# Kernel optimization log

Measured on AMD Instinct MI355X. Metric: run time of the kernel, lower is better.

## Reference

```python
import jax, jax.numpy as jnp
import numpy as np

H, I, E, TOP_K = 2048, 8192, 8, 2
B, S = 2, 2048


def setup_inputs() -> dict:
    key = jax.random.key(0)
    k1, k2, k3, k4 = jax.random.split(key, 4)
    scale_h = 1.0 / np.sqrt(H)
    scale_i = 1.0 / np.sqrt(I)
    return {
        "hidden_states": jax.random.normal(k1, (B, S, H), dtype=jnp.float32),
        "gate_w": jax.random.normal(k2, (H, E), dtype=jnp.float32) * scale_h,
        "w_in": jax.random.normal(k3, (E, H, I), dtype=jnp.float32) * scale_h,
        "w_out": jax.random.normal(k4, (E, I, H), dtype=jnp.float32) * scale_i,
        "bias": jnp.zeros((H,), dtype=jnp.float32),
        "top_k": TOP_K,
    }


def reference(hidden_states, gate_w, w_in, w_out, bias, top_k):
    b, s, h = hidden_states.shape
    x = hidden_states.reshape(-1, h)                      # [T, H]
    num_experts = gate_w.shape[1]

    router_logits = x @ gate_w                            # [T, E]
    probs = jax.nn.softmax(router_logits.astype(jnp.float32), axis=-1)
    routing_weights, selected = jax.lax.top_k(probs, top_k)  # [T, K]
    # normalize_expert_weights=True
    routing_weights = routing_weights / routing_weights.sum(axis=-1, keepdims=True)
    routing_weights = routing_weights.astype(x.dtype)

    # per-token combine weight for each expert (0 if not selected)
    one_hot = jax.nn.one_hot(selected, num_experts, dtype=x.dtype)  # [T, K, E]
    combine = jnp.einsum('tk,tke->te', routing_weights, one_hot)    # [T, E]

    out = jnp.zeros_like(x)
    for e in range(num_experts):  # small fixed expert loop
        hmid = jax.nn.gelu(x @ w_in[e], approximate=False)  # [T, I]
        out = out + combine[:, e:e + 1] * (hmid @ w_out[e])  # [T, H]

    out = out.reshape(b, s, h) + bias
    return out, router_logits
```

## Files before the change

### kernel.cpp

```cpp
#include <hip/hip_runtime.h>
#include <hip/hip_bf16.h>
#include <math.h>

#define T_TOK 4096
#define H_DIM 2048
#define I_DIM 8192
#define N_EXP 8
#define NPAIR 8192

typedef short bf16x8 __attribute__((ext_vector_type(8)));
typedef float f32x4 __attribute__((ext_vector_type(4)));

__device__ __forceinline__ ushort f2bf(float f) {
    union { float f; unsigned u; } v; v.f = f;
    unsigned u = v.u + 0x7fffu + ((v.u >> 16) & 1u);
    return (ushort)(u >> 16);
}

__global__ void k_init(float* __restrict__ out, const float* __restrict__ bias,
                       int* __restrict__ cnts) {
    int gid = blockIdx.x * 256 + threadIdx.x;
    size_t i = (size_t)gid * 4;
    if (i < (size_t)T_TOK * H_DIM) {
        float4 b = *(const float4*)&bias[i & (H_DIM - 1)];
        *(float4*)&out[i] = b;
    }
    if (gid < 16) cnts[gid] = 0;
}

__global__ void k_cvt_x(const float* __restrict__ x, ushort* __restrict__ xb) {
    size_t i = ((size_t)blockIdx.x * 256 + threadIdx.x) * 4;
    float4 v = *(const float4*)&x[i];
    ushort4 o;
    o.x = f2bf(v.x); o.y = f2bf(v.y); o.z = f2bf(v.z); o.w = f2bf(v.w);
    *(ushort4*)&xb[i] = o;
}

__global__ void k_router(const float* __restrict__ x, const float* __restrict__ gw,
                         float* __restrict__ logits, int* __restrict__ sel,
                         float* __restrict__ wts, int* __restrict__ cnt) {
    int t = blockIdx.x;
    int lane = threadIdx.x;
    const float* xr = x + (size_t)t * H_DIM;
    float s[8] = {0, 0, 0, 0, 0, 0, 0, 0};
    for (int h = lane; h < H_DIM; h += 64) {
        float xv = xr[h];
        const float* g = gw + h * 8;
        float4 g0 = *(const float4*)g;
        float4 g1 = *(const float4*)(g + 4);
        s[0] += xv * g0.x; s[1] += xv * g0.y; s[2] += xv * g0.z; s[3] += xv * g0.w;
        s[4] += xv * g1.x; s[5] += xv * g1.y; s[6] += xv * g1.z; s[7] += xv * g1.w;
    }
#pragma unroll
    for (int off = 32; off > 0; off >>= 1) {
#pragma unroll
        for (int e = 0; e < 8; e++) s[e] += __shfl_xor(s[e], off);
    }
    if (lane < 8) logits[t * 8 + lane] = s[lane];
    if (lane == 0) {
        int e0 = 0; float l0 = s[0];
        for (int e = 1; e < 8; e++) if (s[e] > l0) { l0 = s[e]; e0 = e; }
        int e1 = -1; float l1 = -3.0e38f;
        for (int e = 0; e < 8; e++) if (e != e0 && s[e] > l1) { l1 = s[e]; e1 = e; }
        float w0 = 1.0f / (1.0f + expf(l1 - l0));
        float w1 = 1.0f - w0;
        sel[t * 2] = e0; sel[t * 2 + 1] = e1;
        wts[t * 2] = w0; wts[t * 2 + 1] = w1;
        atomicAdd(&cnt[e0], 1);
        atomicAdd(&cnt[e1], 1);
    }
}

__global__ void k_prefix(const int* __restrict__ cnt, int* __restrict__ offs) {
    if (threadIdx.x == 0 && blockIdx.x == 0) {
        int a = 0;
        for (int e = 0; e < N_EXP; e++) { offs[e] = a; a += cnt[e]; }
        offs[N_EXP] = a;
    }
}

__global__ void k_assign(const int* __restrict__ sel, const float* __restrict__ wts,
                         const int* __restrict__ offs, int* __restrict__ cursor,
                         int* __restrict__ rowinfo, float* __restrict__ rowwt) {
    int t = blockIdx.x * 256 + threadIdx.x;
    if (t >= T_TOK) return;
#pragma unroll
    for (int k = 0; k < 2; k++) {
        int e = sel[t * 2 + k];
        int pos = atomicAdd(&cursor[e], 1);
        int row = offs[e] + pos;
        rowinfo[row] = t;
        rowwt[row] = wts[t * 2 + k];
    }
}

template <int KDIM, int NDIM, int MODE>
__global__ __launch_bounds__(256) void k_gemm(
    const ushort* __restrict__ Abase, const float* __restrict__ Bbase,
    void* __restrict__ outp, const int* __restrict__ rowinfo,
    const float* __restrict__ rowwt, const int* __restrict__ offs) {
    const int e = blockIdx.z;
    const int row_start = offs[e], row_end = offs[e + 1];
    const int row0 = row_start + blockIdx.y * 128;
    if (row0 >= row_end) return;
    const int n0 = blockIdx.x * 128;
    const float* B = Bbase + (size_t)e * KDIM * NDIM;

    __shared__ ushort lds_a[128 * 56];
    __shared__ ushort lds_b[128 * 56];

    const int tid = threadIdx.x;
    const int ar = tid & 127;
    const int ak = (tid >> 7) << 4;
    int r = row0 + ar;
    int rc = (r < row_end) ? r : row_start;
    const ushort* a_src;
    if (MODE == 0) a_src = Abase + (size_t)rowinfo[rc] * KDIM + ak;
    else           a_src = Abase + (size_t)rc * KDIM + ak;
    ushort* a_dst = &lds_a[ar * 56 + ak];

    const int bn = (tid & 31) * 4;
    const int bk = (tid >> 5) * 4;
    const float* b_src = B + (size_t)bk * NDIM + (n0 + bn);

    const int lane = tid & 63;
    const int wid = tid >> 6;
    const int wm = (wid & 1) * 64;
    const int wn = (wid >> 1) * 64;
    const int l15 = lane & 15;
    const int q8 = (lane >> 4) * 8;

    f32x4 acc[4][4] = {};

    for (int k0 = 0; k0 < KDIM; k0 += 32) {
        uint4 av0 = *(const uint4*)(a_src + k0);
        uint4 av1 = *(const uint4*)(a_src + k0 + 8);
        const float* bs = b_src + (size_t)k0 * NDIM;
        float4 b0 = *(const float4*)(bs);
        float4 b1 = *(const float4*)(bs + NDIM);
        float4 b2 = *(const float4*)(bs + 2 * (size_t)NDIM);
        float4 b3 = *(const float4*)(bs + 3 * (size_t)NDIM);
        __syncthreads();
        *(uint4*)a_dst = av0;
        *(uint4*)(a_dst + 8) = av1;
        {
            ushort4 p;
            p.x = f2bf(b0.x); p.y = f2bf(b1.x); p.z = f2bf(b2.x); p.w = f2bf(b3.x);
            *(ushort4*)&lds_b[(bn + 0) * 56 + bk] = p;
            p.x = f2bf(b0.y); p.y = f2bf(b1.y); p.z = f2bf(b2.y); p.w = f2bf(b3.y);
            *(ushort4*)&lds_b[(bn + 1) * 56 + bk] = p;
            p.x = f2bf(b0.z); p.y = f2bf(b1.z); p.z = f2bf(b2.z); p.w = f2bf(b3.z);
            *(ushort4*)&lds_b[(bn + 2) * 56 + bk] = p;
            p.x = f2bf(b0.w); p.y = f2bf(b1.w); p.z = f2bf(b2.w); p.w = f2bf(b3.w);
            *(ushort4*)&lds_b[(bn + 3) * 56 + bk] = p;
        }
        __syncthreads();
        bf16x8 af[4], bfr[4];
#pragma unroll
        for (int mt = 0; mt < 4; mt++)
            af[mt] = *(const bf16x8*)&lds_a[(wm + mt * 16 + l15) * 56 + q8];
#pragma unroll
        for (int nt = 0; nt < 4; nt++)
            bfr[nt] = *(const bf16x8*)&lds_b[(wn + nt * 16 + l15) * 56 + q8];
#pragma unroll
        for (int mt = 0; mt < 4; mt++)
#pragma unroll
            for (int nt = 0; nt < 4; nt++)
                acc[mt][nt] = __builtin_amdgcn_mfma_f32_16x16x32_bf16(
                    af[mt], bfr[nt], acc[mt][nt], 0, 0, 0);
    }

    const int qr = (lane >> 4) * 4;
#pragma unroll
    for (int mt = 0; mt < 4; mt++) {
#pragma unroll
        for (int rg = 0; rg < 4; rg++) {
            int rl = wm + mt * 16 + qr + rg;
            int rglob = row0 + rl;
            if (rglob < row_end) {
                if (MODE == 0) {
                    ushort* hm = (ushort*)outp + (size_t)rglob * NDIM + n0 + wn + l15;
#pragma unroll
                    for (int nt = 0; nt < 4; nt++) {
                        float v = acc[mt][nt][rg];
                        v = 0.5f * v * (1.0f + erff(v * 0.70710678118654752f));
                        hm[nt * 16] = f2bf(v);
                    }
                } else {
                    float w = rowwt[rglob];
                    int tok = rowinfo[rglob];
                    float* op = (float*)outp + (size_t)tok * NDIM + n0 + wn + l15;
#pragma unroll
                    for (int nt = 0; nt < 4; nt++)
                        atomicAdd(&op[nt * 16], w * acc[mt][nt][rg]);
                }
            }
        }
    }
}

extern "C" void kernel_launch(void* const* d_in, const int* in_sizes, int n_in,
                              void* d_out, int out_size, void* d_ws, size_t ws_size,
                              hipStream_t stream) {
    const float* x     = (const float*)d_in[0];
    const float* gw    = (const float*)d_in[1];
    const float* w_in  = (const float*)d_in[2];
    const float* w_out = (const float*)d_in[3];
    const float* bias  = (const float*)d_in[4];

    float* out    = (float*)d_out;
    float* logits = out + (size_t)T_TOK * H_DIM;

    char* ws = (char*)d_ws;
    ushort* xb      = (ushort*)(ws);
    ushort* hmid    = (ushort*)(ws + 16777216);
    int*    rowinfo = (int*)  (ws + 150994944);
    float*  rowwt   = (float*)(ws + 151027712);
    int*    sel     = (int*)  (ws + 151060480);
    float*  wts     = (float*)(ws + 151093248);
    int*    cnt     = (int*)  (ws + 151126016);
    int*    offs    = (int*)  (ws + 151126016 + 64);

    hipLaunchKernelGGL(k_init,   dim3(8192), dim3(256), 0, stream, out, bias, cnt);
    hipLaunchKernelGGL(k_cvt_x,  dim3(8192), dim3(256), 0, stream, x, xb);
    hipLaunchKernelGGL(k_router, dim3(4096), dim3(64),  0, stream, x, gw, logits, sel, wts, cnt);
    hipLaunchKernelGGL(k_prefix, dim3(1),    dim3(64),  0, stream, cnt, offs);
    hipLaunchKernelGGL(k_assign, dim3(16),   dim3(256), 0, stream, sel, wts, offs, cnt + 8, rowinfo, rowwt);

    hipLaunchKernelGGL((k_gemm<H_DIM, I_DIM, 0>), dim3(64, 32, 8), dim3(256), 0, stream,
                       xb, w_in, (void*)hmid, rowinfo, rowwt, offs);
    hipLaunchKernelGGL((k_gemm<I_DIM, H_DIM, 1>), dim3(16, 32, 8), dim3(256), 0, stream,
                       hmid, w_out, (void*)out, rowinfo, rowwt, offs);
}
```

Before: 2.418 ms.

## Pre-transpose weights to bf16 and load GEMM tiles via direct global-to-LDS

Adds a transpose-and-convert kernel that writes each expert weight matrix as K-contiguous bf16 into workspace before each GEMM. The GEMM then fetches A and B tiles with global_load_lds straight into an XOR-swizzled LDS layout, replacing register staging, per-element f32-to-bf16 conversion and padded LDS rows. Meant to halve B-operand traffic inside the GEMM and cut VALU work and LDS bank conflicts. In exchange it adds two full passes over the weights each call, needs a much larger workspace (the kernel returns early without running if it is too small), and the loop now has two barriers per k-step with no double buffering.

```diff
diff --git a/kernel.cpp b/kernel.cpp
--- a/kernel.cpp
+++ b/kernel.cpp
@@ -6,7 +6,6 @@
 #define H_DIM 2048
 #define I_DIM 8192
 #define N_EXP 8
-#define NPAIR 8192
 
 typedef short bf16x8 __attribute__((ext_vector_type(8)));
 typedef float f32x4 __attribute__((ext_vector_type(4)));
@@ -15,6 +14,12 @@
     union { float f; unsigned u; } v; v.f = f;
     unsigned u = v.u + 0x7fffu + ((v.u >> 16) & 1u);
     return (ushort)(u >> 16);
+}
+
+__device__ __forceinline__ void gload16(const void* g, void* l) {
+    __builtin_amdgcn_global_load_lds(
+        (const __attribute__((address_space(1))) unsigned*)g,
+        (__attribute__((address_space(3))) unsigned*)l, 16, 0, 0);
 }
 
 __global__ void k_init(float* __restrict__ out, const float* __restrict__ bias,
@@ -94,9 +99,43 @@
     }
 }
 
+template <int R, int C>
+__global__ __launch_bounds__(256) void k_transcvt(const float* __restrict__ in,
+                                                  ushort* __restrict__ outp) {
+    const float* src = in + (size_t)blockIdx.z * R * C;
+    ushort* dst = outp + (size_t)blockIdx.z * R * C;
+    const int c0 = blockIdx.x * 64, r0 = blockIdx.y * 64;
+    __shared__ float tile[64][65];
+    const int t = threadIdx.x;
+    const int tc = (t & 15) * 4;
+    const int tr = t >> 4;
+#pragma unroll
+    for (int i = 0; i < 4; i++) {
+        int r = tr + i * 16;
+        float4 v = *(const float4*)&src[(size_t)(r0 + r) * C + c0 + tc];
+        tile[r][tc] = v.x; tile[r][tc + 1] = v.y;
+        tile[r][tc + 2] = v.z; tile[r][tc + 3] = v.w;
+    }
+    __syncthreads();
+    const int oc = t >> 2;
+    const int ob = (t & 3) * 16;
+    uint4 w0, w1;
+    w0.x = (uint)f2bf(tile[ob + 0][oc]) | ((uint)f2bf(tile[ob + 1][oc]) << 16);
+    w0.y = (uint)f2bf(tile[ob + 2][oc]) | ((uint)f2bf(tile[ob + 3][oc]) << 16);
+    w0.z = (uint)f2bf(tile[ob + 4][oc]) | ((uint)f2bf(tile[ob + 5][oc]) << 16);
+    w0.w = (uint)f2bf(tile[ob + 6][oc]) | ((uint)f2bf(tile[ob + 7][oc]) << 16);
+    w1.x = (uint)f2bf(tile[ob + 8][oc]) | ((uint)f2bf(tile[ob + 9][oc]) << 16);
+    w1.y = (uint)f2bf(tile[ob + 10][oc]) | ((uint)f2bf(tile[ob + 11][oc]) << 16);
+    w1.z = (uint)f2bf(tile[ob + 12][oc]) | ((uint)f2bf(tile[ob + 13][oc]) << 16);
+    w1.w = (uint)f2bf(tile[ob + 14][oc]) | ((uint)f2bf(tile[ob + 15][oc]) << 16);
+    ushort* drow = dst + (size_t)(c0 + oc) * R + r0 + ob;
+    *(uint4*)drow = w0;
+    *(uint4*)(drow + 8) = w1;
+}
+
 template <int KDIM, int NDIM, int MODE>
 __global__ __launch_bounds__(256) void k_gemm(
-    const ushort* __restrict__ Abase, const float* __restrict__ Bbase,
+    const ushort* __restrict__ Abase, const ushort* __restrict__ BtBase,
     void* __restrict__ outp, const int* __restrict__ rowinfo,
     const float* __restrict__ rowwt, const int* __restrict__ offs) {
     const int e = blockIdx.z;
@@ -104,70 +143,71 @@
     const int row0 = row_start + blockIdx.y * 128;
     if (row0 >= row_end) return;
     const int n0 = blockIdx.x * 128;
-    const float* B = Bbase + (size_t)e * KDIM * NDIM;
-
-    __shared__ ushort lds_a[128 * 56];
-    __shared__ ushort lds_b[128 * 56];
+    const ushort* Bt = BtBase + (size_t)e * KDIM * NDIM;
+
+    __shared__ ushort lds_a[128 * 32];
+    __shared__ ushort lds_b[128 * 32];
 
     const int tid = threadIdx.x;
-    const int ar = tid & 127;
-    const int ak = (tid >> 7) << 4;
-    int r = row0 + ar;
-    int rc = (r < row_end) ? r : row_start;
-    const ushort* a_src;
-    if (MODE == 0) a_src = Abase + (size_t)rowinfo[rc] * KDIM + ak;
-    else           a_src = Abase + (size_t)rc * KDIM + ak;
-    ushort* a_dst = &lds_a[ar * 56 + ak];
-
-    const int bn = (tid & 31) * 4;
-    const int bk = (tid >> 5) * 4;
-    const float* b_src = B + (size_t)bk * NDIM + (n0 + bn);
+    const ushort* asrc[2];
+    const ushort* bsrc[2];
+    ushort* adst[2];
+    ushort* bdst[2];
+#pragma unroll
+    for (int i = 0; i < 2; i++) {
+        const int idx = tid + i * 256;
+        const int r = idx >> 2;
+        const int ke = ((((idx & 3) << 4) ^ (((idx >> 3) & 3) << 4)) >> 1);
+        int rg = row0 + r;
+        int rc = (rg < row_end) ? rg : row_start;
+        if (MODE == 0) asrc[i] = Abase + (size_t)rowinfo[rc] * KDIM + ke;
+        else           asrc[i] = Abase + (size_t)rc * KDIM + ke;
+        bsrc[i] = Bt + (size_t)(n0 + r) * KDIM + ke;
+        adst[i] = lds_a + (size_t)idx * 8;
+        bdst[i] = lds_b + (size_t)idx * 8;
+    }
 
     const int lane = tid & 63;
     const int wid = tid >> 6;
     const int wm = (wid & 1) * 64;
     const int wn = (wid >> 1) * 64;
     const int l15 = lane & 15;
-    const int q8 = (lane >> 4) * 8;
+    const int q16 = (lane >> 4) * 16;
+
+    int aoff[4], boff[4];
+#pragma unroll
+    for (int mt = 0; mt < 4; mt++) {
+        int r = wm + mt * 16 + l15;
+        aoff[mt] = (r * 64 + q16) ^ (((r >> 1) & 3) << 4);
+        r = wn + mt * 16 + l15;
+        boff[mt] = (r * 64 + q16) ^ (((r >> 1) & 3) << 4);
+    }
 
     f32x4 acc[4][4] = {};
-
-    for (int k0 = 0; k0 < KDIM; k0 += 32) {
-        uint4 av0 = *(const uint4*)(a_src + k0);
-        uint4 av1 = *(const uint4*)(a_src + k0 + 8);
-        const float* bs = b_src + (size_t)k0 * NDIM;
-        float4 b0 = *(const float4*)(bs);
-        float4 b1 = *(const float4*)(bs + NDIM);
-        float4 b2 = *(const float4*)(bs + 2 * (size_t)NDIM);
-        float4 b3 = *(const float4*)(bs + 3 * (size_t)NDIM);
-        __syncthreads();
-        *(uint4*)a_dst = av0;
-        *(uint4*)(a_dst + 8) = av1;
-        {
-            ushort4 p;
-            p.x = f2bf(b0.x); p.y = f2bf(b1.x); p.z = f2bf(b2.x); p.w = f2bf(b3.x);
-            *(ushort4*)&lds_b[(bn + 0) * 56 + bk] = p;
-            p.x = f2bf(b0.y); p.y = f2bf(b1.y); p.z = f2bf(b2.y); p.w = f2bf(b3.y);
-            *(ushort4*)&lds_b[(bn + 1) * 56 + bk] = p;
-            p.x = f2bf(b0.z); p.y = f2bf(b1.z); p.z = f2bf(b2.z); p.w = f2bf(b3.z);
-            *(ushort4*)&lds_b[(bn + 2) * 56 + bk] = p;
-            p.x = f2bf(b0.w); p.y = f2bf(b1.w); p.z = f2bf(b2.w); p.w = f2bf(b3.w);
-            *(ushort4*)&lds_b[(bn + 3) * 56 + bk] = p;
+    const char* lap = (const char*)lds_a;
+    const char* lbp = (const char*)lds_b;
+
+    for (int ks = 0; ks < KDIM / 32; ks++) {
+#pragma unroll
+        for (int i = 0; i < 2; i++) {
+            gload16(asrc[i], adst[i]);
+            gload16(bsrc[i], bdst[i]);
+            asrc[i] += 32;
+            bsrc[i] += 32;
         }
         __syncthreads();
         bf16x8 af[4], bfr[4];
 #pragma unroll
-        for (int mt = 0; mt < 4; mt++)
-            af[mt] = *(const bf16x8*)&lds_a[(wm + mt * 16 + l15) * 56 + q8];
-#pragma unroll
-        for (int nt = 0; nt < 4; nt++)
-            bfr[nt] = *(const bf16x8*)&lds_b[(wn + nt * 16 + l15) * 56 + q8];
+        for (int mt = 0; mt < 4; mt++) af[mt] = *(const bf16x8*)(lap + aoff[mt]);
+#pragma unroll
+        for (int nt = 0; nt < 4; nt++) bfr[nt] = *(const bf16x8*)(lbp + boff[nt]);
 #pragma unroll
         for (int mt = 0; mt < 4; mt++)
 #pragma unroll
             for (int nt = 0; nt < 4; nt++)
                 acc[mt][nt] = __builtin_amdgcn_mfma_f32_16x16x32_bf16(
                     af[mt], bfr[nt], acc[mt][nt], 0, 0, 0);
+        __syncthreads();
     }
 
     const int qr = (lane >> 4) * 4;
@@ -212,14 +252,17 @@
     float* logits = out + (size_t)T_TOK * H_DIM;
 
     char* ws = (char*)d_ws;
-    ushort* xb      = (ushort*)(ws);
-    ushort* hmid    = (ushort*)(ws + 16777216);
-    int*    rowinfo = (int*)  (ws + 150994944);
-    float*  rowwt   = (float*)(ws + 151027712);
-    int*    sel     = (int*)  (ws + 151060480);
-    float*  wts     = (float*)(ws + 151093248);
-    int*    cnt     = (int*)  (ws + 151126016);
-    int*    offs    = (int*)  (ws + 151126016 + 64);
+    int*    rowinfo = (int*)  (ws);
+    float*  rowwt   = (float*)(ws + 32768);
+    int*    sel     = (int*)  (ws + 65536);
+    float*  wts     = (float*)(ws + 98304);
+    int*    cnt     = (int*)  (ws + 131072);
+    int*    offs    = (int*)  (ws + 131136);
+    ushort* xb      = (ushort*)(ws + 262144);
+    ushort* hmid    = (ushort*)(ws + 17039360);
+    ushort* wt      = (ushort*)(ws + 151257088);
+    const size_t WS_NEEDED = 419692544ull;
+    if (ws_size < WS_NEEDED) return;
 
     hipLaunchKernelGGL(k_init,   dim3(8192), dim3(256), 0, stream, out, bias, cnt);
     hipLaunchKernelGGL(k_cvt_x,  dim3(8192), dim3(256), 0, stream, x, xb);
@@ -227,8 +270,13 @@
     hipLaunchKernelGGL(k_prefix, dim3(1),    dim3(64),  0, stream, cnt, offs);
     hipLaunchKernelGGL(k_assign, dim3(16),   dim3(256), 0, stream, sel, wts, offs, cnt + 8, rowinfo, rowwt);
 
+    hipLaunchKernelGGL((k_transcvt<H_DIM, I_DIM>), dim3(I_DIM / 64, H_DIM / 64, 8), dim3(256),
+                       0, stream, w_in, wt);
     hipLaunchKernelGGL((k_gemm<H_DIM, I_DIM, 0>), dim3(64, 32, 8), dim3(256), 0, stream,
-                       xb, w_in, (void*)hmid, rowinfo, rowwt, offs);
+                       xb, wt, (void*)hmid, rowinfo, rowwt, offs);
+
+    hipLaunchKernelGGL((k_transcvt<I_DIM, H_DIM>), dim3(H_DIM / 64, I_DIM / 64, 8), dim3(256),
+                       0, stream, w_out, wt);
     hipLaunchKernelGGL((k_gemm<I_DIM, H_DIM, 1>), dim3(16, 32, 8), dim3(256), 0, stream,
-                       hmid, w_out, (void*)out, rowinfo, rowwt, offs);
-}
+                       hmid, wt, (void*)out, rowinfo, rowwt, offs);
+}
```

New measurement: 2.111 ms. 1.15x faster.
